# Optimization experiments

Measured on AMD Instinct MI355X. Metric: run time of the kernel, lower is better.

The kernel has to match this reference:

```python
import jax, jax.numpy as jnp
import numpy as np

B = 16384            # number of subgraphs in the batch
NODES_PER_G = 50     # nodes per subgraph
N = B * NODES_PER_G  # total nodes = 819200
L = 3                # num_gcn_layers
EMB = 32             # emb_dim -> repr dim = (1+L)*EMB = 128
REPR = (1 + L) * EMB
PFEAT, FEAT = 1280, 200
P, D, I = 2000, 10000, 20000
RELS = 2


def setup_inputs() -> dict:
    key = jax.random.key(0)
    ks = jax.random.split(key, 16)
    node_repr = jax.random.normal(ks[0], (N, REPR), jnp.float32)
    profeat = jax.random.normal(ks[1], (P, PFEAT), jnp.float32)
    drugfeat = jax.random.normal(ks[2], (D, FEAT), jnp.float32)
    s1p = 1.0 / np.sqrt(PFEAT); s2 = 1.0 / np.sqrt(EMB); s1 = 1.0 / np.sqrt(FEAT)
    W1p = jax.random.normal(ks[3], (PFEAT, EMB), jnp.float32) * s1p
    b1p = jnp.zeros((EMB,), jnp.float32)
    W2p = jax.random.normal(ks[4], (EMB, EMB), jnp.float32) * s2
    b2p = jnp.zeros((EMB,), jnp.float32)
    W1 = jax.random.normal(ks[5], (FEAT, EMB), jnp.float32) * s1
    b1 = jnp.zeros((EMB,), jnp.float32)
    W2 = jax.random.normal(ks[6], (EMB, EMB), jnp.float32) * s2
    b2 = jnp.zeros((EMB,), jnp.float32)
    fc_in = 3 * REPR + 2 * EMB  # 448
    fc_W = jax.random.normal(ks[7], (fc_in, RELS), jnp.float32) / np.sqrt(fc_in)
    fc_b = jnp.zeros((RELS,), jnp.float32)
    # batched-graph structure: contiguous blocks of NODES_PER_G nodes per graph
    graph_ids = (jnp.arange(N, dtype=jnp.int32) // NODES_PER_G).astype(jnp.int32)
    # exactly one head (id==1) and one tail (id==2) node per graph -> their indices
    head_ids = (jnp.arange(B, dtype=jnp.int32) * NODES_PER_G)
    tail_ids = head_ids + 1
    node_idx = jax.random.randint(ks[8], (N,), 0, I, jnp.int32)
    proind = jax.random.randint(ks[9], (I,), 0, P, jnp.int32)
    drugind = jax.random.randint(ks[10], (I,), 0, D, jnp.int32)
    return dict(node_repr=node_repr, profeat=profeat, drugfeat=drugfeat,
                W1p=W1p, b1p=b1p, W2p=W2p, b2p=b2p,
                W1=W1, b1=b1, W2=W2, b2=b2, fc_W=fc_W, fc_b=fc_b,
                graph_ids=graph_ids, head_ids=head_ids, tail_ids=tail_ids,
                node_idx=node_idx, proind=proind, drugind=drugind)


def reference(node_repr, profeat, drugfeat, W1p, b1p, W2p, b2p,
              W1, b1, W2, b2, fc_W, fc_b,
              graph_ids, head_ids, tail_ids, node_idx, proind, drugind):
    # mean_nodes(g, 'repr'): per-graph mean pooling of node reprs
    sums = jax.ops.segment_sum(node_repr, graph_ids, num_segments=B)      # [B, REPR]
    cnts = jax.ops.segment_sum(jnp.ones((node_repr.shape[0],), node_repr.dtype),
                               graph_ids, num_segments=B)                # [B]
    g_out = sums / cnts[:, None]
    # head/tail embedding gathers (id==1 / id==2 nodes)
    head_embs = node_repr[head_ids]                                       # [B, REPR]
    tail_embs = node_repr[tail_ids]                                       # [B, REPR]
    # nested table lookups: profeat[proind[idx[head]]], drugfeat[drugind[idx[tail]]]
    head_feat = profeat[proind[node_idx[head_ids]]]                       # [B, PFEAT]
    tail_feat = drugfeat[drugind[node_idx[tail_ids]]]                     # [B, FEAT]
    # small fuse MLPs (dropout is identity in eval)
    fuse1 = jax.nn.relu(head_feat @ W1p + b1p) @ W2p + b2p                # [B, EMB]
    fuse2 = jax.nn.relu(tail_feat @ W1 + b1) @ W2 + b2                    # [B, EMB]
    g_rep = jnp.concatenate([g_out, head_embs, tail_embs, fuse1, fuse2], axis=1)
    return g_rep @ fc_W + fc_b                                            # [B, RELS]
```

## Files before the change

kernel.cpp:

```cpp
#include <hip/hip_runtime.h>
#include <hip/hip_bf16.h>

#define B_GRAPHS 16384
#define NODES_PER_G 50
#define REPR 128
#define PFEAT 1280
#define FEAT 200
#define EMB 32
#define P_ROWS 2000
#define D_ROWS 10000

#define NPF (P_ROWS / 8)
#define NDF (D_ROWS / 8)
#define NFUSE (NPF + NDF)
#define NPOOL (B_GRAPHS / 4)
#define NTOT (NPOOL + NFUSE)


__global__ __launch_bounds__(256) void merged_kernel(
    const float* __restrict__ nr,
    const float* __restrict__ profeat,
    const float* __restrict__ drugfeat,
    const float* __restrict__ W1p,
    const float* __restrict__ b1p,
    const float* __restrict__ W2p,
    const float* __restrict__ W1,
    const float* __restrict__ b1,
    const float* __restrict__ W2,
    const float* __restrict__ fcW,
    const float* __restrict__ b2p,
    const float* __restrict__ b2,
    float*       __restrict__ f1out,
    float*       __restrict__ f2out,
    float*       __restrict__ out)
{
    const int bid  = blockIdx.x;
    const int Fb  = (int)(((long)bid * NFUSE) / NTOT);
    const int Fb1 = (int)(((long)(bid + 1) * NFUSE) / NTOT);

    if (Fb1 == Fb) {
        const int wid = threadIdx.x >> 6;
        const int l   = threadIdx.x & 63;
        const int col = l & 31;
        const int g   = (bid - Fb) * 4 + wid;

        const float4* nr4 = (const float4*)nr;
        const long base4 = (long)g * (NODES_PER_G * REPR / 4);

        float4 sp = nr4[base4 + l];
        float4 a0, a1;
        a0 = sp;
        a1.x = a1.y = a1.z = a1.w = 0.f;
        #pragma unroll 4
        for (int it = 1; it <= 24; it += 2) {
            float4 f0 = nr4[base4 + (it + 0) * 64 + l];
            float4 f1 = nr4[base4 + (it + 1) * 64 + l];
            a0.x += f0.x; a0.y += f0.y; a0.z += f0.z; a0.w += f0.w;
            a1.x += f1.x; a1.y += f1.y; a1.z += f1.z; a1.w += f1.w;
        }
        float4 pool;
        pool.x = a0.x + a1.x;
        pool.y = a0.y + a1.y;
        pool.z = a0.z + a1.z;
        pool.w = a0.w + a1.w;

        const float4* fcW4 = (const float4*)fcW;
        float4 wg0 = fcW4[col * 2 + 0], wg1 = fcW4[col * 2 + 1];
        float4 wsp0, wsp1;
        float2 fwb;
        float bw;
        if (l < 32) {
            wsp0 = fcW4[64 + col * 2 + 0];
            wsp1 = fcW4[64 + col * 2 + 1];
            fwb  = *(const float2*)(fcW + (384 + col) * 2);
            bw   = b2p[col];
        } else {
            wsp0 = fcW4[128 + col * 2 + 0];
            wsp1 = fcW4[128 + col * 2 + 1];
            fwb  = *(const float2*)(fcW + (416 + col) * 2);
            bw   = b2[col];
        }

        const float inv50 = 1.0f / (float)NODES_PER_G;
        float p0 = inv50 * (pool.x * wg0.x + pool.y * wg0.z + pool.z * wg1.x + pool.w * wg1.z)
                 + sp.x * wsp0.x + sp.y * wsp0.z + sp.z * wsp1.x + sp.w * wsp1.z
                 + bw * fwb.x;
        float p1 = inv50 * (pool.x * wg0.y + pool.y * wg0.w + pool.z * wg1.y + pool.w * wg1.w)
                 + sp.x * wsp0.y + sp.y * wsp0.w + sp.z * wsp1.y + sp.w * wsp1.w
                 + bw * fwb.y;

        for (int m = 32; m >= 1; m >>= 1) {
            p0 += __shfl_xor(p0, m, 64);
            p1 += __shfl_xor(p1, m, 64);
        }
        if (l == 0) {
            out[g * 2 + 0] = p0;
            out[g * 2 + 1] = p1;
        }
    } else if (Fb < NPF) {
        const int grp  = threadIdx.x >> 5;
        const int lane = threadIdx.x & 31;
        const int p = Fb * 8 + grp;
        float m0 = 0.f, m1 = 0.f;
        #pragma unroll
        for (int k = 0; k < 32; ++k) {
            float w = W2p[lane * 32 + k];
            float2 fw = *(const float2*)(fcW + (384 + k) * 2);
            m0 = fmaf(w, fw.x, m0);
            m1 = fmaf(w, fw.y, m1);
        }
        const float4* pf4 = (const float4*)(profeat + (long)p * PFEAT);
        float a0 = 0.f, a1 = 0.f, a2 = 0.f, a3 = 0.f;
        #pragma unroll 4
        for (int q = 0; q < PFEAT / 4; q += 4) {
            float4 f0 = pf4[q], f1 = pf4[q + 1], f2 = pf4[q + 2], f3 = pf4[q + 3];
            int k = q * 4;
            a0 = fmaf(f0.x, W1p[(k + 0) * 32 + lane], a0);
            a0 = fmaf(f0.y, W1p[(k + 1) * 32 + lane], a0);
            a0 = fmaf(f0.z, W1p[(k + 2) * 32 + lane], a0);
            a0 = fmaf(f0.w, W1p[(k + 3) * 32 + lane], a0);
            a1 = fmaf(f1.x, W1p[(k + 4) * 32 + lane], a1);
            a1 = fmaf(f1.y, W1p[(k + 5) * 32 + lane], a1);
            a1 = fmaf(f1.z, W1p[(k + 6) * 32 + lane], a1);
            a1 = fmaf(f1.w, W1p[(k + 7) * 32 + lane], a1);
            a2 = fmaf(f2.x, W1p[(k + 8) * 32 + lane], a2);
            a2 = fmaf(f2.y, W1p[(k + 9) * 32 + lane], a2);
            a2 = fmaf(f2.z, W1p[(k + 10) * 32 + lane], a2);
            a2 = fmaf(f2.w, W1p[(k + 11) * 32 + lane], a2);
            a3 = fmaf(f3.x, W1p[(k + 12) * 32 + lane], a3);
            a3 = fmaf(f3.y, W1p[(k + 13) * 32 + lane], a3);
            a3 = fmaf(f3.z, W1p[(k + 14) * 32 + lane], a3);
            a3 = fmaf(f3.w, W1p[(k + 15) * 32 + lane], a3);
        }
        float h = fmaxf((a0 + a1) + (a2 + a3) + b1p[lane], 0.f);
        float p0 = h * m0, p1 = h * m1;
        for (int m = 16; m >= 1; m >>= 1) {
            p0 += __shfl_xor(p0, m, 32);
            p1 += __shfl_xor(p1, m, 32);
        }
        if (lane == 0) {
            f1out[p * 2 + 0] = p0;
            f1out[p * 2 + 1] = p1;
        }
    } else {
        const int grp  = threadIdx.x >> 5;
        const int lane = threadIdx.x & 31;
        const int d = (Fb - NPF) * 8 + grp;
        float m0 = 0.f, m1 = 0.f;
        #pragma unroll
        for (int k = 0; k < 32; ++k) {
            float w = W2[lane * 32 + k];
            float2 fw = *(const float2*)(fcW + (416 + k) * 2);
            m0 = fmaf(w, fw.x, m0);
            m1 = fmaf(w, fw.y, m1);
        }
        const float4* df4 = (const float4*)(drugfeat + (long)d * FEAT);
        float a0 = 0.f, a1 = 0.f;
        #pragma unroll 5
        for (int q = 0; q < FEAT / 4; q += 2) {
            float4 f0 = df4[q], f1 = df4[q + 1];
            int k = q * 4;
            a0 = fmaf(f0.x, W1[(k + 0) * 32 + lane], a0);
            a0 = fmaf(f0.y, W1[(k + 1) * 32 + lane], a0);
            a0 = fmaf(f0.z, W1[(k + 2) * 32 + lane], a0);
            a0 = fmaf(f0.w, W1[(k + 3) * 32 + lane], a0);
            a1 = fmaf(f1.x, W1[(k + 4) * 32 + lane], a1);
            a1 = fmaf(f1.y, W1[(k + 5) * 32 + lane], a1);
            a1 = fmaf(f1.z, W1[(k + 6) * 32 + lane], a1);
            a1 = fmaf(f1.w, W1[(k + 7) * 32 + lane], a1);
        }
        float h = fmaxf(a0 + a1 + b1[lane], 0.f);
        float p0 = h * m0, p1 = h * m1;
        for (int m = 16; m >= 1; m >>= 1) {
            p0 += __shfl_xor(p0, m, 32);
            p1 += __shfl_xor(p1, m, 32);
        }
        if (lane == 0) {
            f2out[d * 2 + 0] = p0;
            f2out[d * 2 + 1] = p1;
        }
    }
}

__global__ __launch_bounds__(256) void finalize_kernel(
    const int*   __restrict__ head_ids,
    const int*   __restrict__ tail_ids,
    const int*   __restrict__ node_idx,
    const int*   __restrict__ proind,
    const int*   __restrict__ drugind,
    const float* __restrict__ f1out,
    const float* __restrict__ f2out,
    const float* __restrict__ fcb,
    float*       __restrict__ out)
{
    const int g = blockIdx.x * 256 + threadIdx.x;
    if (g >= B_GRAPHS) return;
    const int prow = proind[node_idx[head_ids[g]]];
    const int drow = drugind[node_idx[tail_ids[g]]];
    const float2 f1v = *(const float2*)(f1out + prow * 2);
    const float2 f2v = *(const float2*)(f2out + drow * 2);
    float2 o = *(float2*)(out + g * 2);
    o.x += f1v.x + f2v.x + fcb[0];
    o.y += f1v.y + f2v.y + fcb[1];
    *(float2*)(out + g * 2) = o;
}

extern "C" void kernel_launch(void* const* d_in, const int* in_sizes, int n_in,
                              void* d_out, int out_size, void* d_ws, size_t ws_size,
                              hipStream_t stream) {
    const float* node_repr = (const float*)d_in[0];
    const float* profeat   = (const float*)d_in[1];
    const float* drugfeat  = (const float*)d_in[2];
    const float* W1p       = (const float*)d_in[3];
    const float* b1p       = (const float*)d_in[4];
    const float* W2p       = (const float*)d_in[5];
    const float* b2p       = (const float*)d_in[6];
    const float* W1        = (const float*)d_in[7];
    const float* b1        = (const float*)d_in[8];
    const float* W2        = (const float*)d_in[9];
    const float* b2        = (const float*)d_in[10];
    const float* fc_W      = (const float*)d_in[11];
    const float* fc_b      = (const float*)d_in[12];
    const int* head_ids    = (const int*)d_in[14];
    const int* tail_ids    = (const int*)d_in[15];
    const int* node_idx    = (const int*)d_in[16];
    const int* proind      = (const int*)d_in[17];
    const int* drugind     = (const int*)d_in[18];

    float* f1out = (float*)d_ws;
    float* f2out = (float*)d_ws + 2 * P_ROWS;
    float* out   = (float*)d_out;

    hipLaunchKernelGGL(merged_kernel, dim3(NTOT), dim3(256), 0, stream,
                       node_repr, profeat, drugfeat, W1p, b1p, W2p, W1, b1, W2,
                       fc_W, b2p, b2, f1out, f2out, out);

    hipLaunchKernelGGL(finalize_kernel, dim3(B_GRAPHS / 256), dim3(256), 0, stream,
                       head_ids, tail_ids, node_idx, proind, drugind,
                       f1out, f2out, fc_b, out);
}
```

Measured before the change: 114.5 us.

## Stream pooled node rows through LDS with async global_load_lds double buffering

Replaces the per-lane register loads of each graph's 50x128 node block with asynchronous global-to-LDS loads (global_load_lds), double-buffered per wave in 1280-float chunks. Manual vmcnt waits overlap the next chunk's fetch with summing the current one. This is meant to keep more bytes in flight and hide memory latency in the bandwidth-bound pooling path. In exchange it adds 40 KB of LDS per block, which may cut occupancy, and relies on hand-written waitcnt ordering without a barrier between the LDS write and the per-wave read.

```diff
diff --git a/kernel.cpp b/kernel.cpp
--- a/kernel.cpp
+++ b/kernel.cpp
@@ -16,6 +16,11 @@
 #define NPOOL (B_GRAPHS / 4)
 #define NTOT (NPOOL + NFUSE)
 
+
+#define GLOAD_LDS(gp, lp)                                                     \
+    __builtin_amdgcn_global_load_lds(                                         \
+        (const __attribute__((address_space(1))) float*)(gp),                 \
+        (__attribute__((address_space(3))) float*)(lp), 16, 0, 0)
 
 __global__ __launch_bounds__(256) void merged_kernel(
     const float* __restrict__ nr,
@@ -34,29 +39,51 @@
     float*       __restrict__ f2out,
     float*       __restrict__ out)
 {
-    const int bid  = blockIdx.x;
+    __shared__ float lds[4][2][1280];
+
+    const int bid = blockIdx.x;
     const int Fb  = (int)(((long)bid * NFUSE) / NTOT);
     const int Fb1 = (int)(((long)(bid + 1) * NFUSE) / NTOT);
 
     if (Fb1 == Fb) {
-        const int wid = threadIdx.x >> 6;
+        const int w   = threadIdx.x >> 6;
         const int l   = threadIdx.x & 63;
         const int col = l & 31;
-        const int g   = (bid - Fb) * 4 + wid;
-
-        const float4* nr4 = (const float4*)nr;
-        const long base4 = (long)g * (NODES_PER_G * REPR / 4);
-
-        float4 sp = nr4[base4 + l];
+        const int g   = (bid - Fb) * 4 + w;
+
+        const float* gbase = nr + (long)g * (NODES_PER_G * REPR);
+
+        #pragma unroll
+        for (int c = 0; c < 5; ++c)
+            GLOAD_LDS(gbase + c * 256 + l * 4, &lds[w][0][c * 256]);
+
+        float4 sp;
         float4 a0, a1;
-        a0 = sp;
+        a0.x = a0.y = a0.z = a0.w = 0.f;
         a1.x = a1.y = a1.z = a1.w = 0.f;
-        #pragma unroll 4
-        for (int it = 1; it <= 24; it += 2) {
-            float4 f0 = nr4[base4 + (it + 0) * 64 + l];
-            float4 f1 = nr4[base4 + (it + 1) * 64 + l];
-            a0.x += f0.x; a0.y += f0.y; a0.z += f0.z; a0.w += f0.w;
-            a1.x += f1.x; a1.y += f1.y; a1.z += f1.z; a1.w += f1.w;
+
+        #pragma unroll
+        for (int tt = 0; tt < 5; ++tt) {
+            if (tt < 4) {
+                const float* gt = gbase + (tt + 1) * 1280;
+                #pragma unroll
+                for (int c = 0; c < 5; ++c)
+                    GLOAD_LDS(gt + c * 256 + l * 4, &lds[w][(tt + 1) & 1][c * 256]);
+                asm volatile("s_waitcnt vmcnt(5)" ::: "memory");
+            } else {
+                asm volatile("s_waitcnt vmcnt(0)" ::: "memory");
+            }
+            const float* lb = &lds[w][tt & 1][0];
+            #pragma unroll
+            for (int c = 0; c < 5; ++c) {
+                float4 v = *(const float4*)(lb + c * 256 + l * 4);
+                if (tt == 0 && c == 0) sp = v;
+                if (c & 1) {
+                    a1.x += v.x; a1.y += v.y; a1.z += v.z; a1.w += v.w;
+                } else {
+                    a0.x += v.x; a0.y += v.y; a0.z += v.z; a0.w += v.w;
+                }
+            }
         }
         float4 pool;
         pool.x = a0.x + a1.x;
```

After: 113.8 us. No clear change (-0.7%).
